# Kernel optimization log

Hardware: AMD Instinct MI355X
Metric: run time of the kernel (lower is better)

## Reference

```python
import jax, jax.numpy as jnp
import numpy as np

N_SEGMENT = 8  # frames per clip
N_DIV = 8      # fold divisor: fold = C // N_DIV channels shift each way


def setup_inputs() -> dict:
    key = jax.random.key(0)
    k1, k2 = jax.random.split(key)
    x = jax.random.normal(k1, (128, 256, 28, 28), dtype=jnp.float32)  # [nt, C, H, W], nt = 16 clips * 8 frames
    net_weight = jax.random.normal(k2, (256, 256), dtype=jnp.float32) * 0.0625  # 1x1 conv [out_c, in_c]
    return {"x": x, "net_weight": net_weight}


def temporal_shift(x):
    # x: [nt, C, H, W]. Equivalent to the fixed one-hot depthwise Conv3d (k=3, pad=1):
    #   channels [:fold]        -> out[t] = x[t-1]  (weight[...,0]=1)
    #   channels [fold:2*fold]  -> out[t] = x[t+1]  (weight[...,2]=1)
    #   channels [2*fold:]      -> out[t] = x[t]    (weight[...,1]=1)
    nt, c, h, w = x.shape
    b = nt // N_SEGMENT
    xv = x.reshape(b, N_SEGMENT, c, h, w)
    fold = c // N_DIV
    prev = jnp.pad(xv[:, :-1, :fold], ((0, 0), (1, 0), (0, 0), (0, 0), (0, 0)))       # shift right in time
    nxt = jnp.pad(xv[:, 1:, fold:2 * fold], ((0, 0), (0, 1), (0, 0), (0, 0), (0, 0)))  # shift left in time
    shifted = jnp.concatenate([prev, nxt, xv[:, :, 2 * fold:]], axis=2)
    return shifted.reshape(nt, c, h, w)


def reference(x, net_weight):
    y = temporal_shift(x)
    # wrapped net: 1x1 Conv2d(256 -> 256, bias=False) == per-pixel GEMM
    out = jnp.einsum('nchw,oc->nohw', y, net_weight)
    return out
```

## Files before the change

kernel.cpp:

```cpp
#include <hip/hip_runtime.h>
#include <hip/hip_bf16.h>


#define N_FRAMES 8
#define C_DIM    256
#define HW       784
#define P_TILE   112
#define FOLD     32
#define LDS_STRIDE 264

using bf16x8 = __attribute__((ext_vector_type(8))) short;
using f32x4  = __attribute__((ext_vector_type(4))) float;

static __device__ __forceinline__ unsigned int pk2(float lo, float hi) {
    union { __hip_bfloat162 h; unsigned int u; } cv;
    cv.h = __float22bfloat162_rn(make_float2(lo, hi));
    return cv.u;
}

__global__ void wconv(const float* __restrict__ w, unsigned short* __restrict__ wb) {
    const int i = (blockIdx.x * 256 + threadIdx.x) * 4;
    f32x4 v = *(const f32x4*)(w + i);
    unsigned int lo = pk2(v[0], v[1]);
    unsigned int hi = pk2(v[2], v[3]);
    *(uint2*)(wb + i) = make_uint2(lo, hi);
}

template <bool USE_WB>
__global__ __launch_bounds__(512, 4)
void tsm_pw_gemm(const float* __restrict__ x,
                 const float* __restrict__ w,
                 const unsigned short* __restrict__ wb,
                 float* __restrict__ out) {
    __shared__ __align__(16) unsigned short ylds[P_TILE * LDS_STRIDE];

    const int n    = blockIdx.x;
    const int tile = blockIdx.y;
    const int p0   = tile * P_TILE;
    const int tid  = threadIdx.x;
    const int tf   = n & (N_FRAMES - 1);

    f32x4 v0[7], v1[7];
    int   cps[7], pvs[7];
    #pragma unroll
    for (int i = 0; i < 7; ++i) {
        const int idx = tid + i * 512;
        const int cp  = idx / 28;
        const int pv  = idx - cp * 28;
        cps[i] = cp; pvs[i] = pv;
        const int c0 = cp * 2;
        int  nsrc;
        bool valid;
        if (c0 < FOLD)           { nsrc = n - 1; valid = (tf > 0); }
        else if (c0 < 2 * FOLD)  { nsrc = n + 1; valid = (tf < N_FRAMES - 1); }
        else                     { nsrc = n;     valid = true; }
        const float* src = x + ((size_t)(valid ? nsrc : n) * C_DIM + c0) * HW
                             + p0 + pv * 4;
        f32x4 a = {0.f, 0.f, 0.f, 0.f};
        f32x4 b = {0.f, 0.f, 0.f, 0.f};
        if (valid) {
            a = *(const f32x4*)src;
            b = *(const f32x4*)(src + HW);
        }
        v0[i] = a; v1[i] = b;
    }
    __builtin_amdgcn_sched_barrier(0);
    #pragma unroll
    for (int i = 0; i < 7; ++i) {
        const int c0 = cps[i] * 2;
        const int pv = pvs[i];
        const int cc = c0 ^ ((pv & 7) << 3);
        const int rb = pv * 4 * LDS_STRIDE + cc;
        #pragma unroll
        for (int r = 0; r < 4; ++r)
            *(unsigned int*)&ylds[rb + r * LDS_STRIDE] = pk2(v0[i][r], v1[i][r]);
    }
    __syncthreads();

    const int lane = tid & 63;
    const int wv   = tid >> 6;
    const int g    = lane >> 4;
    const int ol   = lane & 15;

    f32x4 acc[2][7];
    #pragma unroll
    for (int m = 0; m < 2; ++m)
        #pragma unroll
        for (int nn = 0; nn < 7; ++nn)
            acc[m][nn] = f32x4{0.f, 0.f, 0.f, 0.f};

    #pragma unroll
    for (int kk = 0; kk < 8; ++kk) {
        const int c = kk * 32 + g * 8;
        bf16x8 af[2];
        #pragma unroll
        for (int m = 0; m < 2; ++m) {
            const int o = wv * 32 + m * 16 + ol;
            if (USE_WB) {
                af[m] = *(const bf16x8*)&wb[(size_t)o * C_DIM + c];
            } else {
                const float* wp = w + (size_t)o * C_DIM + c;
                f32x4 w0 = *(const f32x4*)wp;
                f32x4 w1 = *(const f32x4*)(wp + 4);
                union { bf16x8 v; unsigned int u4[4]; } cv;
                cv.u4[0] = pk2(w0[0], w0[1]);
                cv.u4[1] = pk2(w0[2], w0[3]);
                cv.u4[2] = pk2(w1[0], w1[1]);
                cv.u4[3] = pk2(w1[2], w1[3]);
                af[m] = cv.v;
            }
        }
        #pragma unroll
        for (int nn = 0; nn < 7; ++nn) {
            const int p  = nn * 16 + ol;
            const int cc = c ^ (((p >> 2) & 7) << 3);
            const bf16x8 bfrag = *(const bf16x8*)&ylds[p * LDS_STRIDE + cc];
            #pragma unroll
            for (int m = 0; m < 2; ++m)
                acc[m][nn] = __builtin_amdgcn_mfma_f32_16x16x32_bf16(
                    af[m], bfrag, acc[m][nn], 0, 0, 0);
        }
    }

    const size_t outbase = (size_t)n * C_DIM * HW + p0 + ol;
    #pragma unroll
    for (int m = 0; m < 2; ++m) {
        #pragma unroll
        for (int r = 0; r < 4; ++r) {
            const int o = wv * 32 + m * 16 + g * 4 + r;
            float* orow = out + outbase + (size_t)o * HW;
            #pragma unroll
            for (int nn = 0; nn < 7; ++nn)
                orow[nn * 16] = acc[m][nn][r];
        }
    }
}

extern "C" void kernel_launch(void* const* d_in, const int* in_sizes, int n_in,
                              void* d_out, int out_size, void* d_ws, size_t ws_size,
                              hipStream_t stream) {
    const float* x = (const float*)d_in[0];
    const float* w = (const float*)d_in[1];
    float* out     = (float*)d_out;
    dim3 grid(128, 7, 1);
    if (ws_size >= (size_t)C_DIM * C_DIM * sizeof(unsigned short)) {
        unsigned short* wb = (unsigned short*)d_ws;
        wconv<<<64, 256, 0, stream>>>(w, wb);
        tsm_pw_gemm<true><<<grid, dim3(512, 1, 1), 0, stream>>>(x, w, wb, out);
    } else {
        tsm_pw_gemm<false><<<grid, dim3(512, 1, 1), 0, stream>>>(x, w, nullptr, out);
    }
}
```

Baseline: 52.32 us.

## Replace one-shot tile GEMM with persistent double-buffered pipelined kernel

Replaces the 896-block grid with 512 persistent blocks that walk 32-pixel tiles. Each block prefetches the next tile's shifted input into registers with inline asm loads while running MFMAs on the current tile, staged through a double-buffered fp32 LDS tile. Invalid temporal-shift reads point at a small zeroed workspace buffer so the loads need no branches. The bf16 conversion of activations moves from the LDS write to the LDS read. The aim is to overlap global-load latency with compute, at the cost of smaller tiles, more weight reloads per tile, an extra memset launch, and uncoalesced strided output stores.

```diff
diff --git a/kernel.cpp b/kernel.cpp
--- a/kernel.cpp
+++ b/kernel.cpp
@@ -2,12 +2,14 @@
 #include <hip/hip_bf16.h>
 
 
-#define N_FRAMES 8
-#define C_DIM    256
-#define HW       784
-#define P_TILE   112
-#define FOLD     32
-#define LDS_STRIDE 264
+#define CDIM 256
+#define HWPX 784
+#define FR_STRIDE (CDIM * HWPX)
+#define QTOT (128 * HWPX)
+#define TPX 32
+#define NTILES (QTOT / TPX)
+#define NBLK 512
+#define LROW 260
 
 using bf16x8 = __attribute__((ext_vector_type(8))) short;
 using f32x4  = __attribute__((ext_vector_type(4))) float;
@@ -21,119 +23,206 @@
 __global__ void wconv(const float* __restrict__ w, unsigned short* __restrict__ wb) {
     const int i = (blockIdx.x * 256 + threadIdx.x) * 4;
     f32x4 v = *(const f32x4*)(w + i);
-    unsigned int lo = pk2(v[0], v[1]);
-    unsigned int hi = pk2(v[2], v[3]);
-    *(uint2*)(wb + i) = make_uint2(lo, hi);
-}
-
-template <bool USE_WB>
+    *(uint2*)(wb + i) = make_uint2(pk2(v[0], v[1]), pk2(v[2], v[3]));
+}
+
 __global__ __launch_bounds__(512, 4)
-void tsm_pw_gemm(const float* __restrict__ x,
-                 const float* __restrict__ w,
-                 const unsigned short* __restrict__ wb,
-                 float* __restrict__ out) {
-    __shared__ __align__(16) unsigned short ylds[P_TILE * LDS_STRIDE];
-
-    const int n    = blockIdx.x;
-    const int tile = blockIdx.y;
-    const int p0   = tile * P_TILE;
+void tsm_pipe(const float* __restrict__ x,
+              const unsigned short* __restrict__ wb,
+              const float* __restrict__ zbuf,
+              float* __restrict__ out) {
+    __shared__ __align__(16) float yb[2][TPX * LROW];
+
     const int tid  = threadIdx.x;
-    const int tf   = n & (N_FRAMES - 1);
-
-    f32x4 v0[7], v1[7];
-    int   cps[7], pvs[7];
-    #pragma unroll
-    for (int i = 0; i < 7; ++i) {
-        const int idx = tid + i * 512;
-        const int cp  = idx / 28;
-        const int pv  = idx - cp * 28;
-        cps[i] = cp; pvs[i] = pv;
-        const int c0 = cp * 2;
-        int  nsrc;
-        bool valid;
-        if (c0 < FOLD)           { nsrc = n - 1; valid = (tf > 0); }
-        else if (c0 < 2 * FOLD)  { nsrc = n + 1; valid = (tf < N_FRAMES - 1); }
-        else                     { nsrc = n;     valid = true; }
-        const float* src = x + ((size_t)(valid ? nsrc : n) * C_DIM + c0) * HW
-                             + p0 + pv * 4;
-        f32x4 a = {0.f, 0.f, 0.f, 0.f};
-        f32x4 b = {0.f, 0.f, 0.f, 0.f};
-        if (valid) {
-            a = *(const f32x4*)src;
-            b = *(const f32x4*)(src + HW);
-        }
-        v0[i] = a; v1[i] = b;
-    }
-    __builtin_amdgcn_sched_barrier(0);
-    #pragma unroll
-    for (int i = 0; i < 7; ++i) {
-        const int c0 = cps[i] * 2;
-        const int pv = pvs[i];
-        const int cc = c0 ^ ((pv & 7) << 3);
-        const int rb = pv * 4 * LDS_STRIDE + cc;
-        #pragma unroll
-        for (int r = 0; r < 4; ++r)
-            *(unsigned int*)&ylds[rb + r * LDS_STRIDE] = pk2(v0[i][r], v1[i][r]);
-    }
-    __syncthreads();
-
     const int lane = tid & 63;
     const int wv   = tid >> 6;
     const int g    = lane >> 4;
     const int ol   = lane & 15;
 
+    const int vp  = tid & 7;
+    const int cb0 = tid >> 3;
+    int  cj[4]; long coff[4]; int dj[4];
+    #pragma unroll
+    for (int j = 0; j < 4; ++j) {
+        const int c = cb0 + j * 64;
+        cj[j]   = c;
+        coff[j] = (long)c * HWPX;
+        dj[j]   = (c < 32) ? -1 : (c < 64 ? 1 : 0);
+    }
+
+    int t   = blockIdx.x;
+    int buf = 0;
+    f32x4 rv[4];
+
+    #define LOADS(TT)                                                          \
+    {                                                                          \
+        const int gp  = (TT) * TPX + vp * 4;                                   \
+        const int nf  = gp / HWPX;                                             \
+        const int pin = gp - nf * HWPX;                                        \
+        const int tf  = nf & 7;                                                \
+        const float* base = x + (size_t)nf * FR_STRIDE + pin;                  \
+        _Pragma("unroll")                                                      \
+        for (int j = 0; j < 4; ++j) {                                          \
+            const bool valid = (dj[j] == 0) ? true                             \
+                             : (dj[j] < 0 ? (tf > 0) : (tf < 7));              \
+            const float* sp = valid ? (base + (long)dj[j] * FR_STRIDE + coff[j])\
+                                    : zbuf;                                    \
+            asm volatile("global_load_dwordx4 %0, %1, off"                     \
+                         : "=v"(rv[j]) : "v"(sp));                             \
+        }                                                                      \
+    }
+
+    #define WRITE_LDS(B)                                                       \
+    {                                                                          \
+        float* d = &yb[(B)][0];                                                \
+        _Pragma("unroll")                                                      \
+        for (int j = 0; j < 4; ++j) {                                          \
+            const int base = (vp * 4) * LROW + cj[j];                          \
+            _Pragma("unroll")                                                  \
+            for (int e = 0; e < 4; ++e) d[base + e * LROW] = rv[j][e];         \
+        }                                                                      \
+    }
+
+    LOADS(t);
+    asm volatile("s_waitcnt vmcnt(0)" ::: "memory");
+    __builtin_amdgcn_sched_barrier(0);
+    WRITE_LDS(0);
+    __syncthreads();
+
+    while (1) {
+        const int  tn   = t + NBLK;
+        const bool more = tn < NTILES;
+        if (more) LOADS(tn);
+
+        f32x4 acc[2][2];
+        #pragma unroll
+        for (int m = 0; m < 2; ++m)
+            #pragma unroll
+            for (int nn = 0; nn < 2; ++nn)
+                acc[m][nn] = f32x4{0.f, 0.f, 0.f, 0.f};
+
+        const float* yr = &yb[buf][0];
+        #pragma unroll
+        for (int kk = 0; kk < 8; ++kk) {
+            const int ca = kk * 32 + g * 8;
+            const bf16x8 af0 = *(const bf16x8*)&wb[(size_t)(wv * 32 + ol) * CDIM + ca];
+            const bf16x8 af1 = *(const bf16x8*)&wb[(size_t)(wv * 32 + 16 + ol) * CDIM + ca];
+            #pragma unroll
+            for (int nn = 0; nn < 2; ++nn) {
+                const int pl = nn * 16 + ol;
+                const float* yp = yr + pl * LROW + ca;
+                const f32x4 y0 = *(const f32x4*)yp;
+                const f32x4 y1 = *(const f32x4*)(yp + 4);
+                union { bf16x8 v; unsigned int u[4]; } cvb;
+                cvb.u[0] = pk2(y0[0], y0[1]);
+                cvb.u[1] = pk2(y0[2], y0[3]);
+                cvb.u[2] = pk2(y1[0], y1[1]);
+                cvb.u[3] = pk2(y1[2], y1[3]);
+                acc[0][nn] = __builtin_amdgcn_mfma_f32_16x16x32_bf16(af0, cvb.v, acc[0][nn], 0, 0, 0);
+                acc[1][nn] = __builtin_amdgcn_mfma_f32_16x16x32_bf16(af1, cvb.v, acc[1][nn], 0, 0, 0);
+            }
+        }
+
+        #pragma unroll
+        for (int nn = 0; nn < 2; ++nn) {
+            const int q  = t * TPX + nn * 16 + ol;
+            const int nf = q / HWPX;
+            const int p  = q - nf * HWPX;
+            float* ob = out + (size_t)nf * FR_STRIDE + p;
+            #pragma unroll
+            for (int m = 0; m < 2; ++m)
+                #pragma unroll
+                for (int r = 0; r < 4; ++r) {
+                    const int o = wv * 32 + m * 16 + g * 4 + r;
+                    ob[(size_t)o * HWPX] = acc[m][nn][r];
+                }
+        }
+
+        if (!more) break;
+        __syncthreads();
+        asm volatile("s_waitcnt vmcnt(16)" ::: "memory");
+        __builtin_amdgcn_sched_barrier(0);
+        WRITE_LDS(buf ^ 1);
+        __syncthreads();
+        buf ^= 1;
+        t = tn;
+    }
+    #undef LOADS
+    #undef WRITE_LDS
+}
+
+#define P_TILE 112
+#define LDS_STRIDE 264
+__global__ __launch_bounds__(512, 4)
+void tsm_fallback(const float* __restrict__ x, const float* __restrict__ w,
+                  float* __restrict__ out) {
+    __shared__ __align__(16) unsigned short ylds[P_TILE * LDS_STRIDE];
+    const int n = blockIdx.x, tile = blockIdx.y, p0 = tile * P_TILE;
+    const int tid = threadIdx.x, tf = n & 7;
+    f32x4 v0[7], v1[7]; int cps[7], pvs[7];
+    #pragma unroll
+    for (int i = 0; i < 7; ++i) {
+        const int idx = tid + i * 512, cp = idx / 28, pv = idx - cp * 28;
+        cps[i] = cp; pvs[i] = pv;
+        const int c0 = cp * 2;
+        int nsrc; bool valid;
+        if (c0 < 32)      { nsrc = n - 1; valid = (tf > 0); }
+        else if (c0 < 64) { nsrc = n + 1; valid = (tf < 7); }
+        else              { nsrc = n;     valid = true; }
+        const float* src = x + ((size_t)(valid ? nsrc : n) * CDIM + c0) * HWPX + p0 + pv * 4;
+        f32x4 a = {0,0,0,0}, b = {0,0,0,0};
+        if (valid) { a = *(const f32x4*)src; b = *(const f32x4*)(src + HWPX); }
+        v0[i] = a; v1[i] = b;
+    }
+    #pragma unroll
+    for (int i = 0; i < 7; ++i) {
+        const int c0 = cps[i] * 2, pv = pvs[i];
+        const int cc = c0 ^ ((pv & 7) << 3);
+        const int rb = pv * 4 * LDS_STRIDE + cc;
+        #pragma unroll
+        for (int r = 0; r < 4; ++r)
+            *(unsigned int*)&ylds[rb + r * LDS_STRIDE] = pk2(v0[i][r], v1[i][r]);
+    }
+    __syncthreads();
+    const int lane = tid & 63, wv = tid >> 6, g = lane >> 4, ol = lane & 15;
     f32x4 acc[2][7];
     #pragma unroll
     for (int m = 0; m < 2; ++m)
         #pragma unroll
-        for (int nn = 0; nn < 7; ++nn)
-            acc[m][nn] = f32x4{0.f, 0.f, 0.f, 0.f};
-
+        for (int nn = 0; nn < 7; ++nn) acc[m][nn] = f32x4{0,0,0,0};
     #pragma unroll
     for (int kk = 0; kk < 8; ++kk) {
         const int c = kk * 32 + g * 8;
         bf16x8 af[2];
         #pragma unroll
         for (int m = 0; m < 2; ++m) {
-            const int o = wv * 32 + m * 16 + ol;
-            if (USE_WB) {
-                af[m] = *(const bf16x8*)&wb[(size_t)o * C_DIM + c];
-            } else {
-                const float* wp = w + (size_t)o * C_DIM + c;
-                f32x4 w0 = *(const f32x4*)wp;
-                f32x4 w1 = *(const f32x4*)(wp + 4);
-                union { bf16x8 v; unsigned int u4[4]; } cv;
-                cv.u4[0] = pk2(w0[0], w0[1]);
-                cv.u4[1] = pk2(w0[2], w0[3]);
-                cv.u4[2] = pk2(w1[0], w1[1]);
-                cv.u4[3] = pk2(w1[2], w1[3]);
-                af[m] = cv.v;
-            }
+            const float* wp = w + (size_t)(wv * 32 + m * 16 + ol) * CDIM + c;
+            f32x4 w0 = *(const f32x4*)wp, w1 = *(const f32x4*)(wp + 4);
+            union { bf16x8 v; unsigned int u4[4]; } cv;
+            cv.u4[0] = pk2(w0[0], w0[1]); cv.u4[1] = pk2(w0[2], w0[3]);
+            cv.u4[2] = pk2(w1[0], w1[1]); cv.u4[3] = pk2(w1[2], w1[3]);
+            af[m] = cv.v;
         }
         #pragma unroll
         for (int nn = 0; nn < 7; ++nn) {
-            const int p  = nn * 16 + ol;
+            const int p = nn * 16 + ol;
             const int cc = c ^ (((p >> 2) & 7) << 3);
-            const bf16x8 bfrag = *(const bf16x8*)&ylds[p * LDS_STRIDE + cc];
+            const bf16x8 bf = *(const bf16x8*)&ylds[p * LDS_STRIDE + cc];
             #pragma unroll
             for (int m = 0; m < 2; ++m)
-                acc[m][nn] = __builtin_amdgcn_mfma_f32_16x16x32_bf16(
-                    af[m], bfrag, acc[m][nn], 0, 0, 0);
-        }
-    }
-
-    const size_t outbase = (size_t)n * C_DIM * HW + p0 + ol;
-    #pragma unroll
-    for (int m = 0; m < 2; ++m) {
+                acc[m][nn] = __builtin_amdgcn_mfma_f32_16x16x32_bf16(af[m], bf, acc[m][nn], 0, 0, 0);
+        }
+    }
+    const size_t outbase = (size_t)n * CDIM * HWPX + p0 + ol;
+    #pragma unroll
+    for (int m = 0; m < 2; ++m)
         #pragma unroll
         for (int r = 0; r < 4; ++r) {
             const int o = wv * 32 + m * 16 + g * 4 + r;
-            float* orow = out + outbase + (size_t)o * HW;
-            #pragma unroll
-            for (int nn = 0; nn < 7; ++nn)
-                orow[nn * 16] = acc[m][nn][r];
-        }
-    }
+            float* orow = out + outbase + (size_t)o * HWPX;
+            #pragma unroll
+            for (int nn = 0; nn < 7; ++nn) orow[nn * 16] = acc[m][nn][r];
+        }
 }
 
 extern "C" void kernel_launch(void* const* d_in, const int* in_sizes, int n_in,
@@ -142,12 +231,14 @@
     const float* x = (const float*)d_in[0];
     const float* w = (const float*)d_in[1];
     float* out     = (float*)d_out;
-    dim3 grid(128, 7, 1);
-    if (ws_size >= (size_t)C_DIM * C_DIM * sizeof(unsigned short)) {
-        unsigned short* wb = (unsigned short*)d_ws;
-        wconv<<<64, 256, 0, stream>>>(w, wb);
-        tsm_pw_gemm<true><<<grid, dim3(512, 1, 1), 0, stream>>>(x, w, wb, out);
+    const size_t wb_bytes = (size_t)CDIM * CDIM * sizeof(unsigned short);
+    if (ws_size >= wb_bytes + 256) {
+        unsigned short* wbuf = (unsigned short*)d_ws;
+        float* zbuf = (float*)((char*)d_ws + wb_bytes);
+        hipMemsetAsync(zbuf, 0, 256, stream);
+        wconv<<<64, 256, 0, stream>>>(w, wbuf);
+        tsm_pipe<<<NBLK, dim3(512, 1, 1), 0, stream>>>(x, wbuf, zbuf, out);
     } else {
-        tsm_pw_gemm<false><<<grid, dim3(512, 1, 1), 0, stream>>>(x, w, nullptr, out);
-    }
-}
+        tsm_fallback<<<dim3(128, 7, 1), dim3(512, 1, 1), 0, stream>>>(x, w, out);
+    }
+}
```

Measured after the change: 81.83 us. +56.4%, slower.
